# Optimization experiments

Measured on AMD Instinct MI355X. Metric: run time of the kernel, lower is better.

The kernel has to match this reference:

```python
import jax, jax.numpy as jnp
import numpy as np

D = 8192  # input dim (len of x_i/x_f)
M = 8192  # output dim (rows of W)


def setup_inputs() -> dict:
    key = jax.random.key(0)
    k = jax.random.split(key, 6)
    return {
        "t": jax.random.uniform(k[0], (), dtype=jnp.float32),
        "y": jax.random.normal(k[1], (M,), dtype=jnp.float32),
        "x_i": jax.random.normal(k[2], (D,), dtype=jnp.float32),
        "x_f": jax.random.normal(k[3], (D,), dtype=jnp.float32),
        "W": jax.random.normal(k[4], (M, D), dtype=jnp.float32) * 0.01,
        "b": jax.random.normal(k[5], (M,), dtype=jnp.float32),
    }


def reference(t, y, x_i, x_f, W, b):
    # grad_y: Jacobian of sigmoid(W x + b) w.r.t. x, evaluated at the
    # pre-update x (self.x == x_i on the first forward call), i.e. diag(s*(1-s)) @ W.
    s = jax.nn.sigmoid(W @ x_i + b)  # [M]
    # Path rectification term: the original loops autograd.grad over each entry of
    # x = (1-t)*x_i + t*x_f; its derivative w.r.t. t is simply x_f - x_i (vectorized).
    v = x_f - x_i  # [D]
    # y_increment = gradient_term @ v = diag(s*(1-s)) W v, fused so the [M, D]
    # Jacobian is never materialized.
    return (s * (1.0 - s)) * (W @ v)  # [M]
```

## Files before the change

kernel.cpp:

```cpp
#include <hip/hip_runtime.h>
#include <math.h>


constexpr int D_DIM = 8192;
constexpr int BLOCK = 1024;
constexpr int ROWS_PER_BLOCK = 16;

__global__ __launch_bounds__(BLOCK)
void dyn_fused_kernel(const float* __restrict__ x_i,
                      const float* __restrict__ x_f,
                      const float* __restrict__ W,
                      const float* __restrict__ b,
                      float* __restrict__ out,
                      int M)
{
    __shared__ float s_xi[D_DIM];
    __shared__ float s_v[D_DIM];

    const int tid = threadIdx.x;
    constexpr int NCHUNK = D_DIM / 4;

    const float4* xi_g = reinterpret_cast<const float4*>(x_i);
    const float4* xf_g = reinterpret_cast<const float4*>(x_f);
    float4* sxi_w = reinterpret_cast<float4*>(s_xi);
    float4* sv_w  = reinterpret_cast<float4*>(s_v);
    #pragma unroll
    for (int c = tid; c < NCHUNK; c += BLOCK) {
        float4 a = xi_g[c];
        float4 f = xf_g[c];
        sxi_w[c] = a;
        sv_w[c]  = make_float4(f.x - a.x, f.y - a.y, f.z - a.z, f.w - a.w);
    }
    __syncthreads();

    const int wave = tid >> 6;
    const int lane = tid & 63;
    const int row  = blockIdx.x * ROWS_PER_BLOCK + wave;
    if (row >= M) return;

    const float4* Wr  = reinterpret_cast<const float4*>(W + (size_t)row * D_DIM);
    const float4* sxi = reinterpret_cast<const float4*>(s_xi);
    const float4* sv  = reinterpret_cast<const float4*>(s_v);

    float acc_i = 0.0f;
    float acc_v = 0.0f;
    #pragma unroll 4
    for (int c = lane; c < NCHUNK; c += 64) {
        float4 w  = Wr[c];
        float4 xi = sxi[c];
        float4 vv = sv[c];
        acc_i = fmaf(w.x, xi.x, acc_i);
        acc_i = fmaf(w.y, xi.y, acc_i);
        acc_i = fmaf(w.z, xi.z, acc_i);
        acc_i = fmaf(w.w, xi.w, acc_i);
        acc_v = fmaf(w.x, vv.x, acc_v);
        acc_v = fmaf(w.y, vv.y, acc_v);
        acc_v = fmaf(w.z, vv.z, acc_v);
        acc_v = fmaf(w.w, vv.w, acc_v);
    }

    #pragma unroll
    for (int off = 32; off > 0; off >>= 1) {
        acc_i += __shfl_down(acc_i, off, 64);
        acc_v += __shfl_down(acc_v, off, 64);
    }

    if (lane == 0) {
        float z = acc_i + b[row];
        float s = 1.0f / (1.0f + expf(-z));
        out[row] = s * (1.0f - s) * acc_v;
    }
}

extern "C" void kernel_launch(void* const* d_in, const int* in_sizes, int n_in,
                              void* d_out, int out_size, void* d_ws, size_t ws_size,
                              hipStream_t stream) {
    const float* x_i = (const float*)d_in[2];
    const float* x_f = (const float*)d_in[3];
    const float* W   = (const float*)d_in[4];
    const float* b   = (const float*)d_in[5];
    float* out = (float*)d_out;
    const int M = out_size;

    const int grid = (M + ROWS_PER_BLOCK - 1) / ROWS_PER_BLOCK;
    dyn_fused_kernel<<<grid, BLOCK, 0, stream>>>(x_i, x_f, W, b, out, M);
}
```

Measured before the change: 48.66 us.

## Drop LDS staging of x vectors, compute W·x_f and derive W·v algebraically

```diff
diff --git a/kernel.cpp b/kernel.cpp
--- a/kernel.cpp
+++ b/kernel.cpp
@@ -3,10 +3,12 @@
 
 
 constexpr int D_DIM = 8192;
-constexpr int BLOCK = 1024;
-constexpr int ROWS_PER_BLOCK = 16;
+constexpr int BLOCK = 256;
+constexpr int ROWS_PER_BLOCK = 4;
+constexpr int NCHUNK = D_DIM / 4;
+constexpr int KPW = NCHUNK / 64;
 
-__global__ __launch_bounds__(BLOCK)
+__global__ __launch_bounds__(BLOCK, 8)
 void dyn_fused_kernel(const float* __restrict__ x_i,
                       const float* __restrict__ x_f,
                       const float* __restrict__ W,
@@ -14,61 +16,44 @@
                       float* __restrict__ out,
                       int M)
 {
-    __shared__ float s_xi[D_DIM];
-    __shared__ float s_v[D_DIM];
-
-    const int tid = threadIdx.x;
-    constexpr int NCHUNK = D_DIM / 4;
-
-    const float4* xi_g = reinterpret_cast<const float4*>(x_i);
-    const float4* xf_g = reinterpret_cast<const float4*>(x_f);
-    float4* sxi_w = reinterpret_cast<float4*>(s_xi);
-    float4* sv_w  = reinterpret_cast<float4*>(s_v);
-    #pragma unroll
-    for (int c = tid; c < NCHUNK; c += BLOCK) {
-        float4 a = xi_g[c];
-        float4 f = xf_g[c];
-        sxi_w[c] = a;
-        sv_w[c]  = make_float4(f.x - a.x, f.y - a.y, f.z - a.z, f.w - a.w);
-    }
-    __syncthreads();
-
+    const int tid  = threadIdx.x;
     const int wave = tid >> 6;
     const int lane = tid & 63;
     const int row  = blockIdx.x * ROWS_PER_BLOCK + wave;
     if (row >= M) return;
 
     const float4* Wr  = reinterpret_cast<const float4*>(W + (size_t)row * D_DIM);
-    const float4* sxi = reinterpret_cast<const float4*>(s_xi);
-    const float4* sv  = reinterpret_cast<const float4*>(s_v);
+    const float4* xi4 = reinterpret_cast<const float4*>(x_i);
+    const float4* xf4 = reinterpret_cast<const float4*>(x_f);
 
     float acc_i = 0.0f;
-    float acc_v = 0.0f;
+    float acc_f = 0.0f;
     #pragma unroll 4
-    for (int c = lane; c < NCHUNK; c += 64) {
+    for (int k = 0; k < KPW; ++k) {
+        const int c = lane + k * 64;
         float4 w  = Wr[c];
-        float4 xi = sxi[c];
-        float4 vv = sv[c];
+        float4 xi = xi4[c];
+        float4 xf = xf4[c];
         acc_i = fmaf(w.x, xi.x, acc_i);
         acc_i = fmaf(w.y, xi.y, acc_i);
         acc_i = fmaf(w.z, xi.z, acc_i);
         acc_i = fmaf(w.w, xi.w, acc_i);
-        acc_v = fmaf(w.x, vv.x, acc_v);
-        acc_v = fmaf(w.y, vv.y, acc_v);
-        acc_v = fmaf(w.z, vv.z, acc_v);
-        acc_v = fmaf(w.w, vv.w, acc_v);
+        acc_f = fmaf(w.x, xf.x, acc_f);
+        acc_f = fmaf(w.y, xf.y, acc_f);
+        acc_f = fmaf(w.z, xf.z, acc_f);
+        acc_f = fmaf(w.w, xf.w, acc_f);
     }
 
     #pragma unroll
     for (int off = 32; off > 0; off >>= 1) {
         acc_i += __shfl_down(acc_i, off, 64);
-        acc_v += __shfl_down(acc_v, off, 64);
+        acc_f += __shfl_down(acc_f, off, 64);
     }
 
     if (lane == 0) {
         float z = acc_i + b[row];
         float s = 1.0f / (1.0f + expf(-z));
-        out[row] = s * (1.0f - s) * acc_v;
+        out[row] = s * (1.0f - s) * (acc_f - acc_i);
     }
 }
 
```

Result: faster. 44.04 us (-9.5%).
